# Optimization experiments

Measured on AMD Instinct MI355X. Metric: run time of the kernel, lower is better.

## Reference

```python
import jax, jax.numpy as jnp
import numpy as np

N_POINTS = 1_000_000
FDIM = 32
GRID = 128  # gx = gy = gz = ceil(20 / 0.15625) = 128
LO, HI = -10.0, 10.0
INIT_STD = 0.05


def setup_inputs() -> dict:
    key = jax.random.key(0)
    k1, k2 = jax.random.split(key)
    # query points inside the bound
    x = jax.random.uniform(k1, (N_POINTS, 3), jnp.float32, LO, HI)
    # dense voxel feature grid, layout [C, D, H, W] (squeezed batch dim)
    feature = jax.random.normal(k2, (FDIM, GRID, GRID, GRID), jnp.float32) * INIT_STD
    return {"x": x, "feature": feature}


def reference(x, feature):
    # normalize_coordinates: map bound -> [-1, 1] per axis (x, y, z order)
    coords = 2.0 * (x - LO) / (HI - LO) - 1.0  # [N, 3]

    C, D, H, W = feature.shape
    # grid_sample, align_corners=False: pixel = ((c + 1) * size - 1) / 2
    fx = ((coords[:, 0] + 1.0) * W - 1.0) * 0.5
    fy = ((coords[:, 1] + 1.0) * H - 1.0) * 0.5
    fz = ((coords[:, 2] + 1.0) * D - 1.0) * 0.5

    x0f, y0f, z0f = jnp.floor(fx), jnp.floor(fy), jnp.floor(fz)
    wx, wy, wz = fx - x0f, fy - y0f, fz - z0f  # trilinear fractions
    x0 = x0f.astype(jnp.int32)
    y0 = y0f.astype(jnp.int32)
    z0 = z0f.astype(jnp.int32)

    feat_flat = feature.reshape(C, -1)  # [C, D*H*W]
    out = jnp.zeros((C, x.shape[0]), dtype=feature.dtype)
    for dz in (0, 1):
        for dy in (0, 1):
            for dx in (0, 1):
                xi, yi, zi = x0 + dx, y0 + dy, z0 + dz
                w = ((wx if dx else 1.0 - wx)
                     * (wy if dy else 1.0 - wy)
                     * (wz if dz else 1.0 - wz))
                # padding_mode='zeros': out-of-range corners contribute 0
                valid = ((xi >= 0) & (xi < W) & (yi >= 0) & (yi < H)
                         & (zi >= 0) & (zi < D))
                idx = ((jnp.clip(zi, 0, D - 1) * H + jnp.clip(yi, 0, H - 1)) * W
                       + jnp.clip(xi, 0, W - 1))
                vals = feat_flat[:, idx]  # gather -> [C, N]
                out = out + vals * (w * valid).astype(feature.dtype)[None, :]
    # transpose(0, 1) -> [N, fdim]
    return out.T
```

## Files before the change

kernel.cpp:

```cpp
#include <hip/hip_runtime.h>


constexpr int   GD      = 128;
constexpr long long SPATIAL = (long long)GD * GD * GD;
constexpr int   FD      = 32;
constexpr float PLO     = -10.0f;
constexpr float PHI     = 10.0f;

__global__ __launch_bounds__(256) void transpose_feat(
    const float* __restrict__ f, float* __restrict__ o) {
    __shared__ float lds[64][FD + 1];
    const int t  = threadIdx.x;
    const int s0 = blockIdx.x * 64;
    const int sl = t & 63;
    const int cq = t >> 6;
#pragma unroll
    for (int it = 0; it < 8; ++it) {
        const int c = it * 4 + cq;
        lds[sl][c] = f[(size_t)c * SPATIAL + s0 + sl];
    }
    __syncthreads();
    const int cw  = t & 31;
    const int swb = t >> 5;
#pragma unroll
    for (int it = 0; it < 8; ++it) {
        const int s = swb + it * 8;
        o[(size_t)(s0 + s) * FD + cw] = lds[s][cw];
    }
}

__global__ __launch_bounds__(256) void trilerp(
    const float* __restrict__ x, const float* __restrict__ ft,
    float* __restrict__ out, int npts) {
    const int tid = blockIdx.x * 256 + threadIdx.x;
    const int n = tid >> 3;
    if (n >= npts) return;
    const int j = tid & 7;

    const float px = x[3 * n + 0];
    const float py = x[3 * n + 1];
    const float pz = x[3 * n + 2];

    const float cx = 2.0f * (px - PLO) / (PHI - PLO) - 1.0f;
    const float cy = 2.0f * (py - PLO) / (PHI - PLO) - 1.0f;
    const float cz = 2.0f * (pz - PLO) / (PHI - PLO) - 1.0f;
    const float fx = ((cx + 1.0f) * GD - 1.0f) * 0.5f;
    const float fy = ((cy + 1.0f) * GD - 1.0f) * 0.5f;
    const float fz = ((cz + 1.0f) * GD - 1.0f) * 0.5f;

    const float x0f = floorf(fx), y0f = floorf(fy), z0f = floorf(fz);
    const float wx = fx - x0f, wy = fy - y0f, wz = fz - z0f;
    const int x0 = (int)x0f, y0 = (int)y0f, z0 = (int)z0f;

    float4 acc = make_float4(0.f, 0.f, 0.f, 0.f);
#pragma unroll
    for (int dz = 0; dz < 2; ++dz) {
#pragma unroll
        for (int dy = 0; dy < 2; ++dy) {
#pragma unroll
            for (int dx = 0; dx < 2; ++dx) {
                const int xi = x0 + dx, yi = y0 + dy, zi = z0 + dz;
                const bool valid = ((unsigned)xi < (unsigned)GD) &
                                   ((unsigned)yi < (unsigned)GD) &
                                   ((unsigned)zi < (unsigned)GD);
                float w = (dx ? wx : 1.0f - wx) * (dy ? wy : 1.0f - wy) *
                          (dz ? wz : 1.0f - wz);
                w = valid ? w : 0.0f;
                const int xc = min(max(xi, 0), GD - 1);
                const int yc = min(max(yi, 0), GD - 1);
                const int zc = min(max(zi, 0), GD - 1);
                const size_t idx = (size_t)(zc * GD + yc) * GD + xc;
                const float4 v =
                    *reinterpret_cast<const float4*>(ft + idx * FD + j * 4);
                acc.x = fmaf(v.x, w, acc.x);
                acc.y = fmaf(v.y, w, acc.y);
                acc.z = fmaf(v.z, w, acc.z);
                acc.w = fmaf(v.w, w, acc.w);
            }
        }
    }
    *reinterpret_cast<float4*>(out + (size_t)n * FD + j * 4) = acc;
}

__global__ __launch_bounds__(256) void trilerp_direct(
    const float* __restrict__ x, const float* __restrict__ f,
    float* __restrict__ out, int npts) {
    const int tid = blockIdx.x * 256 + threadIdx.x;
    const int n = tid >> 3;
    if (n >= npts) return;
    const int j = tid & 7;

    const float px = x[3 * n + 0];
    const float py = x[3 * n + 1];
    const float pz = x[3 * n + 2];
    const float cx = 2.0f * (px - PLO) / (PHI - PLO) - 1.0f;
    const float cy = 2.0f * (py - PLO) / (PHI - PLO) - 1.0f;
    const float cz = 2.0f * (pz - PLO) / (PHI - PLO) - 1.0f;
    const float fx = ((cx + 1.0f) * GD - 1.0f) * 0.5f;
    const float fy = ((cy + 1.0f) * GD - 1.0f) * 0.5f;
    const float fz = ((cz + 1.0f) * GD - 1.0f) * 0.5f;
    const float x0f = floorf(fx), y0f = floorf(fy), z0f = floorf(fz);
    const float wx = fx - x0f, wy = fy - y0f, wz = fz - z0f;
    const int x0 = (int)x0f, y0 = (int)y0f, z0 = (int)z0f;

    float acc[4] = {0.f, 0.f, 0.f, 0.f};
#pragma unroll
    for (int dz = 0; dz < 2; ++dz)
#pragma unroll
        for (int dy = 0; dy < 2; ++dy)
#pragma unroll
            for (int dx = 0; dx < 2; ++dx) {
                const int xi = x0 + dx, yi = y0 + dy, zi = z0 + dz;
                const bool valid = ((unsigned)xi < (unsigned)GD) &
                                   ((unsigned)yi < (unsigned)GD) &
                                   ((unsigned)zi < (unsigned)GD);
                float w = (dx ? wx : 1.0f - wx) * (dy ? wy : 1.0f - wy) *
                          (dz ? wz : 1.0f - wz);
                w = valid ? w : 0.0f;
                const int xc = min(max(xi, 0), GD - 1);
                const int yc = min(max(yi, 0), GD - 1);
                const int zc = min(max(zi, 0), GD - 1);
                const size_t idx = (size_t)(zc * GD + yc) * GD + xc;
#pragma unroll
                for (int k = 0; k < 4; ++k)
                    acc[k] = fmaf(f[(size_t)(j * 4 + k) * SPATIAL + idx], w, acc[k]);
            }
#pragma unroll
    for (int k = 0; k < 4; ++k) out[(size_t)n * FD + j * 4 + k] = acc[k];
}

extern "C" void kernel_launch(void* const* d_in, const int* in_sizes, int n_in,
                              void* d_out, int out_size, void* d_ws, size_t ws_size,
                              hipStream_t stream) {
    const float* x    = (const float*)d_in[0];
    const float* feat = (const float*)d_in[1];
    float*       out  = (float*)d_out;
    const int npts = in_sizes[0] / 3;

    const size_t need = (size_t)SPATIAL * FD * sizeof(float);
    const int gblocks = (npts * 8 + 255) / 256;

    if (ws_size >= need) {
        float* ft = (float*)d_ws;
        transpose_feat<<<(int)(SPATIAL / 64), 256, 0, stream>>>(feat, ft);
        trilerp<<<gblocks, 256, 0, stream>>>(x, ft, out, npts);
    } else {
        trilerp_direct<<<gblocks, 256, 0, stream>>>(x, feat, out, npts);
    }
}
```

Measured before the change: 571.8 us.

## Store transposed feature grid in fp16 and gather half-precision corners

The transpose kernel now writes the channel-last feature grid as fp16 instead of fp32, halving the workspace written and the bytes gathered per corner. The trilerp kernel assigns 4 threads per point, each loading 8 halves (16 bytes) per corner and converting them to float before accumulating. The input read in the transpose and the output store in trilerp use nontemporal hints. Precision drops to fp16 for features (std 0.05), which may or may not stay within tolerance.

```diff
diff --git a/kernel.cpp b/kernel.cpp
--- a/kernel.cpp
+++ b/kernel.cpp
@@ -1,4 +1,5 @@
 #include <hip/hip_runtime.h>
+#include <hip/hip_fp16.h>
 
 
 constexpr int   GD      = 128;
@@ -7,35 +8,41 @@
 constexpr float PLO     = -10.0f;
 constexpr float PHI     = 10.0f;
 
-__global__ __launch_bounds__(256) void transpose_feat(
-    const float* __restrict__ f, float* __restrict__ o) {
+typedef float nfloat4 __attribute__((ext_vector_type(4)));
+
+__global__ __launch_bounds__(256) void transpose_feat_h(
+    const float* __restrict__ f, __half* __restrict__ o) {
     __shared__ float lds[64][FD + 1];
     const int t  = threadIdx.x;
-    const int s0 = blockIdx.x * 64;
+    const long long s0 = (long long)blockIdx.x * 64;
     const int sl = t & 63;
     const int cq = t >> 6;
 #pragma unroll
     for (int it = 0; it < 8; ++it) {
         const int c = it * 4 + cq;
-        lds[sl][c] = f[(size_t)c * SPATIAL + s0 + sl];
+        lds[sl][c] =
+            __builtin_nontemporal_load(f + (size_t)c * SPATIAL + s0 + sl);
     }
     __syncthreads();
-    const int cw  = t & 31;
-    const int swb = t >> 5;
+    const int c0 = (t & 15) * 2;
+    const int sw = t >> 4;
 #pragma unroll
-    for (int it = 0; it < 8; ++it) {
-        const int s = swb + it * 8;
-        o[(size_t)(s0 + s) * FD + cw] = lds[s][cw];
+    for (int it = 0; it < 4; ++it) {
+        const int s = sw + it * 16;
+        __half2 h;
+        h.x = __float2half(lds[s][c0]);
+        h.y = __float2half(lds[s][c0 + 1]);
+        *reinterpret_cast<__half2*>(o + (size_t)(s0 + s) * FD + c0) = h;
     }
 }
 
-__global__ __launch_bounds__(256) void trilerp(
-    const float* __restrict__ x, const float* __restrict__ ft,
+__global__ __launch_bounds__(256) void trilerp_h(
+    const float* __restrict__ x, const __half* __restrict__ ft,
     float* __restrict__ out, int npts) {
     const int tid = blockIdx.x * 256 + threadIdx.x;
-    const int n = tid >> 3;
+    const int n = tid >> 2;
     if (n >= npts) return;
-    const int j = tid & 7;
+    const int j = tid & 3;
 
     const float px = x[3 * n + 0];
     const float py = x[3 * n + 1];
@@ -52,7 +59,7 @@
     const float wx = fx - x0f, wy = fy - y0f, wz = fz - z0f;
     const int x0 = (int)x0f, y0 = (int)y0f, z0 = (int)z0f;
 
-    float4 acc = make_float4(0.f, 0.f, 0.f, 0.f);
+    float acc[8] = {0.f, 0.f, 0.f, 0.f, 0.f, 0.f, 0.f, 0.f};
 #pragma unroll
     for (int dz = 0; dz < 2; ++dz) {
 #pragma unroll
@@ -70,16 +77,23 @@
                 const int yc = min(max(yi, 0), GD - 1);
                 const int zc = min(max(zi, 0), GD - 1);
                 const size_t idx = (size_t)(zc * GD + yc) * GD + xc;
-                const float4 v =
-                    *reinterpret_cast<const float4*>(ft + idx * FD + j * 4);
-                acc.x = fmaf(v.x, w, acc.x);
-                acc.y = fmaf(v.y, w, acc.y);
-                acc.z = fmaf(v.z, w, acc.z);
-                acc.w = fmaf(v.w, w, acc.w);
+                const nfloat4 raw = *reinterpret_cast<const nfloat4*>(
+                    ft + idx * FD + j * 8);
+                const __half2* h2 = reinterpret_cast<const __half2*>(&raw);
+#pragma unroll
+                for (int k = 0; k < 4; ++k) {
+                    const float2 fv = __half22float2(h2[k]);
+                    acc[2 * k + 0] = fmaf(fv.x, w, acc[2 * k + 0]);
+                    acc[2 * k + 1] = fmaf(fv.y, w, acc[2 * k + 1]);
+                }
             }
         }
     }
-    *reinterpret_cast<float4*>(out + (size_t)n * FD + j * 4) = acc;
+    float* op = out + (size_t)n * FD + j * 8;
+    nfloat4 o0 = {acc[0], acc[1], acc[2], acc[3]};
+    nfloat4 o1 = {acc[4], acc[5], acc[6], acc[7]};
+    __builtin_nontemporal_store(o0, reinterpret_cast<nfloat4*>(op));
+    __builtin_nontemporal_store(o1, reinterpret_cast<nfloat4*>(op) + 1);
 }
 
 __global__ __launch_bounds__(256) void trilerp_direct(
@@ -137,14 +151,15 @@
     float*       out  = (float*)d_out;
     const int npts = in_sizes[0] / 3;
 
-    const size_t need = (size_t)SPATIAL * FD * sizeof(float);
-    const int gblocks = (npts * 8 + 255) / 256;
+    const size_t need = (size_t)SPATIAL * FD * sizeof(__half);
 
     if (ws_size >= need) {
-        float* ft = (float*)d_ws;
-        transpose_feat<<<(int)(SPATIAL / 64), 256, 0, stream>>>(feat, ft);
-        trilerp<<<gblocks, 256, 0, stream>>>(x, ft, out, npts);
+        __half* fth = (__half*)d_ws;
+        transpose_feat_h<<<(int)(SPATIAL / 64), 256, 0, stream>>>(feat, fth);
+        const int gblocks = (npts * 4 + 255) / 256;
+        trilerp_h<<<gblocks, 256, 0, stream>>>(x, fth, out, npts);
     } else {
+        const int gblocks = (npts * 8 + 255) / 256;
         trilerp_direct<<<gblocks, 256, 0, stream>>>(x, feat, out, npts);
     }
 }
```

New measurement: 497.7 us. -13.0%, faster.
